# Optimization experiments

Hardware: AMD Instinct MI355X
Metric: run time of the kernel (lower is better)

## Reference

```python
import jax, jax.numpy as jnp
import numpy as np

NUM_ATOMS = 100000
NUM_BONDS = 200000
MAX_NB = 6
ATOM_FDIM = 133
BOND_FDIM = 147
HIDDEN = 300
DEPTH = 4
NUM_MOLS = 8192


def setup_inputs() -> dict:
    key = jax.random.key(0)
    ks = jax.random.split(key, 10)
    f_atoms = jax.random.normal(ks[0], (NUM_ATOMS, ATOM_FDIM), dtype=jnp.float32)
    f_bonds = jax.random.normal(ks[1], (NUM_BONDS, BOND_FDIM), dtype=jnp.float32)
    a2b = jax.random.randint(ks[2], (NUM_ATOMS, MAX_NB), 0, NUM_BONDS, dtype=jnp.int32)
    b2a = jax.random.randint(ks[3], (NUM_BONDS,), 0, NUM_ATOMS, dtype=jnp.int32)
    b2revb = jax.random.randint(ks[4], (NUM_BONDS,), 0, NUM_BONDS, dtype=jnp.int32)
    mol_ids = jnp.sort(jax.random.randint(ks[5], (NUM_ATOMS,), 0, NUM_MOLS, dtype=jnp.int32))
    s = 1.0 / np.sqrt(HIDDEN)
    W_i = jax.random.uniform(ks[6], (BOND_FDIM, HIDDEN), jnp.float32, -s, s)
    W_h = jax.random.uniform(ks[7], (HIDDEN, HIDDEN), jnp.float32, -s, s)
    W_o = jax.random.uniform(ks[8], (ATOM_FDIM + HIDDEN, HIDDEN), jnp.float32, -s, s)
    b_o = jax.random.uniform(ks[9], (HIDDEN,), jnp.float32, -s, s)
    return {"f_atoms": f_atoms, "f_bonds": f_bonds, "W_i": W_i, "W_h": W_h,
            "W_o": W_o, "b_o": b_o, "a2b": a2b, "b2a": b2a, "b2revb": b2revb,
            "mol_ids": mol_ids}


def reference(f_atoms, f_bonds, W_i, W_h, W_o, b_o, a2b, b2a, b2revb, mol_ids):
    # initial bond messages: W_i then activation (bias=False)
    inp = f_bonds @ W_i                       # [B, H]
    message = jax.nn.relu(inp)
    for _ in range(DEPTH - 1):
        nei = message[a2b]                    # [A, MAX_NB, H] gather
        a_message = nei.sum(axis=1)           # [A, H]
        rev_message = message[b2revb]         # [B, H]
        message = a_message[b2a] - rev_message
        message = jax.nn.relu(inp + message @ W_h)
    # final atom readout
    a_message = message[a2b].sum(axis=1)      # [A, H]
    a_input = jnp.concatenate([f_atoms, a_message], axis=1)
    atom_hiddens = jax.nn.relu(a_input @ W_o + b_o)
    # per-molecule mean aggregation (== chemprop a_scope loop with 'mean')
    sums = jax.ops.segment_sum(atom_hiddens, mol_ids, num_segments=NUM_MOLS)
    counts = jax.ops.segment_sum(jnp.ones((NUM_ATOMS,), jnp.float32), mol_ids,
                                 num_segments=NUM_MOLS)
    return sums / jnp.maximum(counts, 1.0)[:, None]
```

## Files before the change

### kernel.cpp

```cpp
#include <hip/hip_runtime.h>


#define DEVFN static __device__ __forceinline__

typedef __attribute__((ext_vector_type(8))) __bf16 bf16x8;
typedef __attribute__((ext_vector_type(4))) float floatx4;

DEVFN unsigned short f2bf(float f) {
    unsigned int u = __float_as_uint(f);
    u += 0x7FFFu + ((u >> 16) & 1u);
    return (unsigned short)(u >> 16);
}
DEVFN float bf2f(unsigned int u) { return __uint_as_float(u << 16); }

DEVFN unsigned int bfsub2(unsigned int a, unsigned int m) {
    float lo = bf2f(a & 0xffffu) - bf2f(m & 0xffffu);
    float hi = bf2f(a >> 16) - bf2f(m >> 16);
    return (unsigned int)f2bf(lo) | ((unsigned int)f2bf(hi) << 16);
}
DEVFN uint4 bfsub8(uint4 a, uint4 m) {
    return make_uint4(bfsub2(a.x, m.x), bfsub2(a.y, m.y),
                      bfsub2(a.z, m.z), bfsub2(a.w, m.w));
}

__global__ __launch_bounds__(256) void dbg_fill(float* out, int n, float v) {
    int t = blockIdx.x * 256 + threadIdx.x;
    if (t < n) out[t] = v;
}

__global__ __launch_bounds__(256) void prep_wih(const float* __restrict__ Wi,
                                                const float* __restrict__ Wh,
                                                unsigned short* __restrict__ Wt) {
    int t = blockIdx.x * 256 + threadIdx.x;
    if (t >= 320 * 480) return;
    int n = t / 480, k = t - n * 480;
    float v = 0.f;
    if (n < 300) {
        if (k < 147) v = Wi[k * 300 + n];
        else if (k >= 160 && k < 460) v = Wh[(k - 160) * 300 + n];
    }
    Wt[t] = f2bf(v);
}

__global__ __launch_bounds__(256) void prep_wto(const float* __restrict__ Wo,
                                                unsigned short* __restrict__ Wt) {
    int t = blockIdx.x * 256 + threadIdx.x;
    if (t >= 320 * 448) return;
    int n = t / 448, k = t - n * 448;
    float v = 0.f;
    if (n < 300) {
        if (k < 300) v = Wo[(133 + k) * 300 + n];
        else if (k >= 304 && k < 437) v = Wo[(k - 304) * 300 + n];
    }
    Wt[t] = f2bf(v);
}

__global__ __launch_bounds__(256) void pad_bonds(const float* __restrict__ fb,
                                                 unsigned short* __restrict__ out) {
    int t = blockIdx.x * 256 + threadIdx.x;
    if (t >= 200000 * 20) return;
    int b = t / 20, c = t - b * 20;
    unsigned int o[4];
#pragma unroll
    for (int p = 0; p < 4; ++p) {
        int sc = c * 8 + p * 2;
        float v0 = (sc < 147) ? fb[(size_t)b * 147 + sc] : 0.f;
        float v1 = (sc + 1 < 147) ? fb[(size_t)b * 147 + sc + 1] : 0.f;
        o[p] = (unsigned int)f2bf(v0) | ((unsigned int)f2bf(v1) << 16);
    }
    *(uint4*)(out + (size_t)b * 160 + c * 8) = make_uint4(o[0], o[1], o[2], o[3]);
}

__global__ __launch_bounds__(256) void atoms_concat(const float* __restrict__ fa,
                                                    unsigned short* __restrict__ concat) {
    int t = blockIdx.x * 256 + threadIdx.x;
    if (t >= 100000 * 18) return;
    int a = t / 18, c = t - a * 18;
    unsigned int o[4];
#pragma unroll
    for (int p = 0; p < 4; ++p) {
        int sc = c * 8 + p * 2;
        float v0 = (sc < 133) ? fa[(size_t)a * 133 + sc] : 0.f;
        float v1 = (sc + 1 < 133) ? fa[(size_t)a * 133 + sc + 1] : 0.f;
        o[p] = (unsigned int)f2bf(v0) | ((unsigned int)f2bf(v1) << 16);
    }
    *(uint4*)(concat + (size_t)a * 448 + 304 + c * 8) = make_uint4(o[0], o[1], o[2], o[3]);
}

template <int CH>
__global__ __launch_bounds__(256) void gather_sum(const unsigned short* __restrict__ msg,
                                                  const int* __restrict__ a2b,
                                                  unsigned short* __restrict__ out,
                                                  int ostride, int nA) {
    int t = blockIdx.x * 256 + threadIdx.x;
    if (t >= nA * CH) return;
    int a = t / CH, c = t - a * CH;
    float s[8] = {0, 0, 0, 0, 0, 0, 0, 0};
#pragma unroll
    for (int j = 0; j < 6; ++j) {
        int b = a2b[a * 6 + j];
        uint4 v = *(const uint4*)(msg + (size_t)b * 320 + c * 8);
        s[0] += bf2f(v.x & 0xffffu); s[1] += bf2f(v.x >> 16);
        s[2] += bf2f(v.y & 0xffffu); s[3] += bf2f(v.y >> 16);
        s[4] += bf2f(v.z & 0xffffu); s[5] += bf2f(v.z >> 16);
        s[6] += bf2f(v.w & 0xffffu); s[7] += bf2f(v.w >> 16);
    }
    unsigned int o[4];
#pragma unroll
    for (int p = 0; p < 4; ++p)
        o[p] = (unsigned int)f2bf(s[2 * p]) | ((unsigned int)f2bf(s[2 * p + 1]) << 16);
    *(uint4*)(out + (size_t)a * ostride + c * 8) = make_uint4(o[0], o[1], o[2], o[3]);
}

template <int KT0, int KT1, int MODE, int BSTRIDE>
__global__ __launch_bounds__(256) void gemm_k(const unsigned short* __restrict__ A0,
                                              int a0s,
                                              const unsigned short* __restrict__ amsg,
                                              const unsigned short* __restrict__ msg,
                                              const int* __restrict__ b2a,
                                              const int* __restrict__ b2revb,
                                              const unsigned short* __restrict__ Wt,
                                              unsigned short* __restrict__ outp,
                                              float* __restrict__ hid,
                                              const float* __restrict__ bo, int M) {
    constexpr int KT = KT0 + KT1;
    __shared__ unsigned short As[2 * 5120];
    __shared__ unsigned short Bs[2 * 5120];

    const int tid = threadIdx.x;
    const int lane = tid & 63;
    const int wave = tid >> 6;
    const int wm = wave & 1, wn = wave >> 1;
    const int l16 = lane & 15, quad = lane >> 4;

    int m0, n0;
    {
        const int bid = blockIdx.x;
        const int MB = (int)(gridDim.x >> 1);
        const int mfull = (MB >> 3) << 3;
        const int FULL = mfull << 1;
        int mb, nh;
        if (bid < FULL) {
            nh = (bid >> 3) & 1;
            mb = ((bid >> 4) << 3) + (bid & 7);
        } else {
            const int r = bid - FULL;
            const int rem = MB - mfull;
            nh = (r >= rem) ? 1 : 0;
            mb = mfull + r - nh * rem;
        }
        m0 = mb * 128;
        n0 = nh * 160;
    }

    const int arow = tid >> 1, ahalf = tid & 1;
    const int gr = min(m0 + arow, M - 1);
    const unsigned short* a0p = A0 + (size_t)gr * a0s + ahalf * 16;
    const unsigned short* a1p = nullptr;
    const unsigned short* m1p = nullptr;
    if (KT1 > 0) {
        a1p = amsg + (size_t)b2a[gr] * 320 + ahalf * 16;
        m1p = msg + (size_t)b2revb[gr] * 320 + ahalf * 16;
    }
    const int u0 = tid, u1 = tid + 256, u2 = tid + 512;
    const unsigned short* bg0 = Wt + (size_t)(n0 + (u0 >> 2)) * BSTRIDE + ((u0 ^ (u0 >> 2)) & 3) * 8;
    const unsigned short* bg1 = Wt + (size_t)(n0 + (u1 >> 2)) * BSTRIDE + ((u1 ^ (u1 >> 2)) & 3) * 8;
    const unsigned short* bg2 = (tid < 128)
        ? Wt + (size_t)(n0 + (u2 >> 2)) * BSTRIDE + ((u2 ^ (u2 >> 2)) & 3) * 8 : Wt;

    int aoff[4], boff[5];
#pragma unroll
    for (int tm = 0; tm < 4; ++tm)
        aoff[tm] = (wm * 64 + tm * 16 + l16) * 40 + quad * 8;
#pragma unroll
    for (int tn = 0; tn < 5; ++tn) {
        int nl = wn * 80 + tn * 16 + l16;
        boff[tn] = nl * 32 + ((quad ^ nl) & 3) * 8;
    }

    floatx4 acc[4][5];
#pragma unroll
    for (int tm = 0; tm < 4; ++tm)
#pragma unroll
        for (int tn = 0; tn < 5; ++tn) acc[tm][tn] = (floatx4){0.f, 0.f, 0.f, 0.f};

    uint4 ar0, ar1, br0, br1, br2;
    auto ldG = [&](int kt) {
        if (kt < KT0) {
            ar0 = *(const uint4*)(a0p + kt * 32);
            ar1 = *(const uint4*)(a0p + kt * 32 + 8);
        } else {
            int ko = (kt - KT0) * 32;
            uint4 va0 = *(const uint4*)(a1p + ko);
            uint4 va1 = *(const uint4*)(a1p + ko + 8);
            uint4 vm0 = *(const uint4*)(m1p + ko);
            uint4 vm1 = *(const uint4*)(m1p + ko + 8);
            ar0 = bfsub8(va0, vm0);
            ar1 = bfsub8(va1, vm1);
        }
        br0 = *(const uint4*)(bg0 + kt * 32);
        br1 = *(const uint4*)(bg1 + kt * 32);
        if (tid < 128) br2 = *(const uint4*)(bg2 + kt * 32);
    };
    auto stW = [&](int buf) {
        unsigned short* ab = As + buf * 5120 + arow * 40 + ahalf * 16;
        *(uint4*)(ab) = ar0;
        *(uint4*)(ab + 8) = ar1;
        unsigned short* bb = Bs + buf * 5120;
        *(uint4*)(bb + u0 * 8) = br0;
        *(uint4*)(bb + u1 * 8) = br1;
        if (tid < 128) *(uint4*)(bb + u2 * 8) = br2;
    };

    ldG(0);
    stW(0);
    __syncthreads();

#pragma unroll
    for (int kt = 0; kt < KT; ++kt) {
        const int buf = kt & 1;
        if (kt + 1 < KT) ldG(kt + 1);

        bf16x8 av[4], bv[5];
#pragma unroll
        for (int tm = 0; tm < 4; ++tm)
            av[tm] = *(const bf16x8*)(As + buf * 5120 + aoff[tm]);
#pragma unroll
        for (int tn = 0; tn < 5; ++tn)
            bv[tn] = *(const bf16x8*)(Bs + buf * 5120 + boff[tn]);
#pragma unroll
        for (int tn = 0; tn < 5; ++tn)
#pragma unroll
            for (int tm = 0; tm < 4; ++tm)
                acc[tm][tn] = __builtin_amdgcn_mfma_f32_16x16x32_bf16(av[tm], bv[tn], acc[tm][tn], 0, 0, 0);

        if (kt + 1 < KT) stW(buf ^ 1);
        __syncthreads();
    }

    float bias[5];
    if (MODE == 2) {
#pragma unroll
        for (int tn = 0; tn < 5; ++tn) {
            int col = n0 + wn * 80 + tn * 16 + l16;
            bias[tn] = (col < 300) ? bo[col] : 0.f;
        }
    }
#pragma unroll
    for (int tm = 0; tm < 4; ++tm) {
        const int r0 = m0 + wm * 64 + tm * 16 + quad * 4;
#pragma unroll
        for (int tn = 0; tn < 5; ++tn) {
            const int col = n0 + wn * 80 + tn * 16 + l16;
#pragma unroll
            for (int i = 0; i < 4; ++i) {
                int r = r0 + i;
                if (r >= M) continue;
                float c = acc[tm][tn][i];
                if (MODE == 2) {
                    if (col < 300) hid[(size_t)r * 300 + col] = fmaxf(c + bias[tn], 0.f);
                } else {
                    outp[(size_t)r * 320 + col] = f2bf(fmaxf(c, 0.f));
                }
            }
        }
    }
}

__global__ __launch_bounds__(320) void mean_k(const float* __restrict__ hid,
                                              const int* __restrict__ mol_ids,
                                              float* __restrict__ out, int nA) {
    int mol = blockIdx.x;
    int lo, hi;
    {
        int l = 0, h = nA;
        while (l < h) { int m = (l + h) >> 1; if (mol_ids[m] < mol) l = m + 1; else h = m; }
        lo = l;
    }
    {
        int l = lo, h = nA;
        while (l < h) { int m = (l + h) >> 1; if (mol_ids[m] < mol + 1) l = m + 1; else h = m; }
        hi = l;
    }
    int col = threadIdx.x;
    if (col >= 300) return;
    float s = 0.f;
    for (int a = lo; a < hi; ++a) s += hid[(size_t)a * 300 + col];
    int cnt = hi - lo;
    out[(size_t)mol * 300 + col] = s / (float)(cnt > 0 ? cnt : 1);
}

extern "C" void kernel_launch(void* const* d_in, const int* in_sizes, int n_in,
                              void* d_out, int out_size, void* d_ws, size_t ws_size,
                              hipStream_t stream) {
    (void)in_sizes; (void)n_in;
    const float* f_atoms = (const float*)d_in[0];
    const float* f_bonds = (const float*)d_in[1];
    const float* W_i     = (const float*)d_in[2];
    const float* W_h     = (const float*)d_in[3];
    const float* W_o     = (const float*)d_in[4];
    const float* b_o     = (const float*)d_in[5];
    const int*   a2b     = (const int*)d_in[6];
    const int*   b2a     = (const int*)d_in[7];
    const int*   b2revb  = (const int*)d_in[8];
    const int*   mol_ids = (const int*)d_in[9];

    const size_t sz_wih  = 320ull * 480 * 2;
    const size_t sz_wto  = 320ull * 448 * 2;
    const size_t sz_fbp  = 200000ull * 160 * 2;
    const size_t sz_amsg = 100000ull * 320 * 2;
    const size_t sz_msg  = 200000ull * 320 * 2;
    const size_t need = sz_wih + sz_wto + sz_fbp + sz_amsg + 2 * sz_msg;

    if (ws_size < need) {
        dbg_fill<<<(out_size + 255) / 256, 256, 0, stream>>>(
            (float*)d_out, out_size, (float)(ws_size >> 20));
        return;
    }

    char* ws = (char*)d_ws;
    unsigned short* wih  = (unsigned short*)(ws);
    unsigned short* wto  = (unsigned short*)(ws + sz_wih);
    unsigned short* fbp  = (unsigned short*)(ws + sz_wih + sz_wto);
    unsigned short* amsg = (unsigned short*)(ws + sz_wih + sz_wto + sz_fbp);
    unsigned short* msgA = (unsigned short*)(ws + sz_wih + sz_wto + sz_fbp + sz_amsg);
    unsigned short* msgB = (unsigned short*)(ws + sz_wih + sz_wto + sz_fbp + sz_amsg + sz_msg);
    unsigned short* concat = msgA;
    float*          hid    = (float*)msgB;

    prep_wih<<<600, 256, 0, stream>>>(W_i, W_h, wih);
    prep_wto<<<560, 256, 0, stream>>>(W_o, wto);
    pad_bonds<<<15625, 256, 0, stream>>>(f_bonds, fbp);

    gemm_k<5, 0, 0, 480><<<dim3(3126), 256, 0, stream>>>(
        fbp, 160, nullptr, nullptr, nullptr, nullptr, wih, msgA, nullptr, nullptr, 200000);

    unsigned short* cur = msgA;
    unsigned short* other = msgB;
    for (int d = 0; d < 3; ++d) {
        gather_sum<40><<<15625, 256, 0, stream>>>(cur, a2b, amsg, 320, 100000);
        gemm_k<5, 10, 0, 480><<<dim3(3126), 256, 0, stream>>>(
            fbp, 160, amsg, cur, b2a, b2revb, wih, other, nullptr, nullptr, 200000);
        unsigned short* t = cur; cur = other; other = t;
    }

    gather_sum<38><<<14844, 256, 0, stream>>>(cur, a2b, concat, 448, 100000);
    atoms_concat<<<7032, 256, 0, stream>>>(f_atoms, concat);
    gemm_k<14, 0, 2, 448><<<dim3(1564), 256, 0, stream>>>(
        concat, 448, nullptr, nullptr, nullptr, nullptr, wto, nullptr, hid, b_o, 100000);
    mean_k<<<8192, 320, 0, stream>>>(hid, mol_ids, (float*)d_out, 100000);
}
```

Measured before the change: 1.167 ms.

## Prefetch global tiles two steps ahead with ping-pong registers in GEMM loop

Deepens the GEMM main-loop software pipeline. Global loads for tile kt+2 are issued into a second register set while tile kt is computed from LDS, so more memory latency is hidden. The __syncthreads is replaced by an explicit lgkmcnt wait, sched barriers and s_barrier. It also drops the trailing barrier after the last tile. This costs extra VGPRs for the second register set, which may lower occupancy.

```diff
diff --git a/kernel.cpp b/kernel.cpp
--- a/kernel.cpp
+++ b/kernel.cpp
@@ -184,43 +184,43 @@
 #pragma unroll
         for (int tn = 0; tn < 5; ++tn) acc[tm][tn] = (floatx4){0.f, 0.f, 0.f, 0.f};
 
-    uint4 ar0, ar1, br0, br1, br2;
-    auto ldG = [&](int kt) {
+    uint4 pa0, pa1, pb0, pb1, pb2;
+    uint4 qa0, qa1, qb0, qb1, qb2;
+
+    auto ldg = [&](int kt, uint4& x0, uint4& x1, uint4& y0, uint4& y1, uint4& y2) {
         if (kt < KT0) {
-            ar0 = *(const uint4*)(a0p + kt * 32);
-            ar1 = *(const uint4*)(a0p + kt * 32 + 8);
+            x0 = *(const uint4*)(a0p + kt * 32);
+            x1 = *(const uint4*)(a0p + kt * 32 + 8);
         } else {
             int ko = (kt - KT0) * 32;
             uint4 va0 = *(const uint4*)(a1p + ko);
             uint4 va1 = *(const uint4*)(a1p + ko + 8);
             uint4 vm0 = *(const uint4*)(m1p + ko);
             uint4 vm1 = *(const uint4*)(m1p + ko + 8);
-            ar0 = bfsub8(va0, vm0);
-            ar1 = bfsub8(va1, vm1);
-        }
-        br0 = *(const uint4*)(bg0 + kt * 32);
-        br1 = *(const uint4*)(bg1 + kt * 32);
-        if (tid < 128) br2 = *(const uint4*)(bg2 + kt * 32);
+            x0 = bfsub8(va0, vm0);
+            x1 = bfsub8(va1, vm1);
+        }
+        y0 = *(const uint4*)(bg0 + kt * 32);
+        y1 = *(const uint4*)(bg1 + kt * 32);
+        if (tid < 128) y2 = *(const uint4*)(bg2 + kt * 32);
     };
-    auto stW = [&](int buf) {
+    auto stw = [&](int buf, const uint4& x0, const uint4& x1,
+                   const uint4& y0, const uint4& y1, const uint4& y2) {
         unsigned short* ab = As + buf * 5120 + arow * 40 + ahalf * 16;
-        *(uint4*)(ab) = ar0;
-        *(uint4*)(ab + 8) = ar1;
+        *(uint4*)(ab) = x0;
+        *(uint4*)(ab + 8) = x1;
         unsigned short* bb = Bs + buf * 5120;
-        *(uint4*)(bb + u0 * 8) = br0;
-        *(uint4*)(bb + u1 * 8) = br1;
-        if (tid < 128) *(uint4*)(bb + u2 * 8) = br2;
+        *(uint4*)(bb + u0 * 8) = y0;
+        *(uint4*)(bb + u1 * 8) = y1;
+        if (tid < 128) *(uint4*)(bb + u2 * 8) = y2;
     };
-
-    ldG(0);
-    stW(0);
-    __syncthreads();
-
-#pragma unroll
-    for (int kt = 0; kt < KT; ++kt) {
-        const int buf = kt & 1;
-        if (kt + 1 < KT) ldG(kt + 1);
-
+    auto barsync = [&]() {
+        asm volatile("s_waitcnt lgkmcnt(0)" ::: "memory");
+        __builtin_amdgcn_sched_barrier(0);
+        __builtin_amdgcn_s_barrier();
+        __builtin_amdgcn_sched_barrier(0);
+    };
+    auto compute = [&](int buf) {
         bf16x8 av[4], bv[5];
 #pragma unroll
         for (int tm = 0; tm < 4; ++tm)
@@ -233,9 +233,24 @@
 #pragma unroll
             for (int tm = 0; tm < 4; ++tm)
                 acc[tm][tn] = __builtin_amdgcn_mfma_f32_16x16x32_bf16(av[tm], bv[tn], acc[tm][tn], 0, 0, 0);
-
-        if (kt + 1 < KT) stW(buf ^ 1);
-        __syncthreads();
+    };
+
+    ldg(0, pa0, pa1, pb0, pb1, pb2);
+    if (KT > 1) ldg(1, qa0, qa1, qb0, qb1, qb2);
+    stw(0, pa0, pa1, pb0, pb1, pb2);
+    barsync();
+
+#pragma unroll
+    for (int kt = 0; kt < KT; ++kt) {
+        if ((kt & 1) == 0) {
+            if (kt + 2 < KT) ldg(kt + 2, pa0, pa1, pb0, pb1, pb2);
+            compute(0);
+            if (kt + 1 < KT) { stw(1, qa0, qa1, qb0, qb1, qb2); barsync(); }
+        } else {
+            if (kt + 2 < KT) ldg(kt + 2, qa0, qa1, qb0, qb1, qb2);
+            compute(1);
+            if (kt + 1 < KT) { stw(0, pa0, pa1, pb0, pb1, pb2); barsync(); }
+        }
     }
 
     float bias[5];
```

After: 1.128 ms. 1.03x faster.

## Load GEMM operands directly into registers, drop LDS staging and fold subtraction into MFMA

Applied to the files above, without the earlier changes.

The GEMM kernel no longer stages A and B tiles through shared memory with barriers. Each wave now loads its MFMA fragments straight from global memory into registers, with a two-deep register prefetch. The a_message minus rev_message subtraction is no longer done in fp32 before bf16 rounding; instead the rev message is sign-flipped and pushed through a second MFMA pass, which doubles MFMA work on the message K-tiles. The launch bounds also request 2 blocks per CU. This removes LDS traffic and syncs, but gives up data reuse across waves (each weight row is fetched by several waves), raises register pressure, and changes the rounding of the subtraction.

```diff
diff --git a/kernel.cpp b/kernel.cpp
--- a/kernel.cpp
+++ b/kernel.cpp
@@ -13,14 +13,9 @@
 }
 DEVFN float bf2f(unsigned int u) { return __uint_as_float(u << 16); }
 
-DEVFN unsigned int bfsub2(unsigned int a, unsigned int m) {
-    float lo = bf2f(a & 0xffffu) - bf2f(m & 0xffffu);
-    float hi = bf2f(a >> 16) - bf2f(m >> 16);
-    return (unsigned int)f2bf(lo) | ((unsigned int)f2bf(hi) << 16);
-}
-DEVFN uint4 bfsub8(uint4 a, uint4 m) {
-    return make_uint4(bfsub2(a.x, m.x), bfsub2(a.y, m.y),
-                      bfsub2(a.z, m.z), bfsub2(a.w, m.w));
+DEVFN uint4 negbf8(uint4 a) {
+    return make_uint4(a.x ^ 0x80008000u, a.y ^ 0x80008000u,
+                      a.z ^ 0x80008000u, a.w ^ 0x80008000u);
 }
 
 __global__ __launch_bounds__(256) void dbg_fill(float* out, int n, float v) {
@@ -113,19 +108,17 @@
 }
 
 template <int KT0, int KT1, int MODE, int BSTRIDE>
-__global__ __launch_bounds__(256) void gemm_k(const unsigned short* __restrict__ A0,
-                                              int a0s,
-                                              const unsigned short* __restrict__ amsg,
-                                              const unsigned short* __restrict__ msg,
-                                              const int* __restrict__ b2a,
-                                              const int* __restrict__ b2revb,
-                                              const unsigned short* __restrict__ Wt,
-                                              unsigned short* __restrict__ outp,
-                                              float* __restrict__ hid,
-                                              const float* __restrict__ bo, int M) {
+__global__ __launch_bounds__(256, 2) void gemm_k(const unsigned short* __restrict__ A0,
+                                                 int a0s,
+                                                 const unsigned short* __restrict__ amsg,
+                                                 const unsigned short* __restrict__ msg,
+                                                 const int* __restrict__ b2a,
+                                                 const int* __restrict__ b2revb,
+                                                 const unsigned short* __restrict__ Wt,
+                                                 unsigned short* __restrict__ outp,
+                                                 float* __restrict__ hid,
+                                                 const float* __restrict__ bo, int M) {
     constexpr int KT = KT0 + KT1;
-    __shared__ unsigned short As[2 * 5120];
-    __shared__ unsigned short Bs[2 * 5120];
 
     const int tid = threadIdx.x;
     const int lane = tid & 63;
@@ -153,89 +146,83 @@
         n0 = nh * 160;
     }
 
-    const int arow = tid >> 1, ahalf = tid & 1;
-    const int gr = min(m0 + arow, M - 1);
-    const unsigned short* a0p = A0 + (size_t)gr * a0s + ahalf * 16;
-    const unsigned short* a1p = nullptr;
-    const unsigned short* m1p = nullptr;
-    if (KT1 > 0) {
-        a1p = amsg + (size_t)b2a[gr] * 320 + ahalf * 16;
-        m1p = msg + (size_t)b2revb[gr] * 320 + ahalf * 16;
-    }
-    const int u0 = tid, u1 = tid + 256, u2 = tid + 512;
-    const unsigned short* bg0 = Wt + (size_t)(n0 + (u0 >> 2)) * BSTRIDE + ((u0 ^ (u0 >> 2)) & 3) * 8;
-    const unsigned short* bg1 = Wt + (size_t)(n0 + (u1 >> 2)) * BSTRIDE + ((u1 ^ (u1 >> 2)) & 3) * 8;
-    const unsigned short* bg2 = (tid < 128)
-        ? Wt + (size_t)(n0 + (u2 >> 2)) * BSTRIDE + ((u2 ^ (u2 >> 2)) & 3) * 8 : Wt;
-
-    int aoff[4], boff[5];
+    const unsigned short* pA0[4];
+    const unsigned short* pA1[4];
+    const unsigned short* pM1[4];
+#pragma unroll
+    for (int tm = 0; tm < 4; ++tm) {
+        const int r = min(m0 + wm * 64 + tm * 16 + l16, M - 1);
+        pA0[tm] = A0 + (size_t)r * a0s + quad * 8;
+        if constexpr (KT1 > 0) {
+            pA1[tm] = amsg + (size_t)b2a[r] * 320 + quad * 8;
+            pM1[tm] = msg + (size_t)b2revb[r] * 320 + quad * 8;
+        } else {
+            pA1[tm] = A0; pM1[tm] = A0;
+        }
+    }
+    const unsigned short* pB[5];
+#pragma unroll
+    for (int tn = 0; tn < 5; ++tn)
+        pB[tn] = Wt + (size_t)(n0 + wn * 80 + tn * 16 + l16) * BSTRIDE + quad * 8;
+
+    floatx4 acc[4][5];
 #pragma unroll
     for (int tm = 0; tm < 4; ++tm)
-        aoff[tm] = (wm * 64 + tm * 16 + l16) * 40 + quad * 8;
-#pragma unroll
-    for (int tn = 0; tn < 5; ++tn) {
-        int nl = wn * 80 + tn * 16 + l16;
-        boff[tn] = nl * 32 + ((quad ^ nl) & 3) * 8;
-    }
-
-    floatx4 acc[4][5];
-#pragma unroll
-    for (int tm = 0; tm < 4; ++tm)
 #pragma unroll
         for (int tn = 0; tn < 5; ++tn) acc[tm][tn] = (floatx4){0.f, 0.f, 0.f, 0.f};
 
-    uint4 ar0, ar1, br0, br1, br2;
-    auto ldG = [&](int kt) {
+    uint4 aP[4], mP[4], bP[5];
+    uint4 aQ[4], mQ[4], bQ[5];
+
+    auto ldg = [&](int kt, uint4 (&a)[4], uint4 (&m)[4], uint4 (&b)[5]) {
         if (kt < KT0) {
-            ar0 = *(const uint4*)(a0p + kt * 32);
-            ar1 = *(const uint4*)(a0p + kt * 32 + 8);
+#pragma unroll
+            for (int tm = 0; tm < 4; ++tm)
+                a[tm] = *(const uint4*)(pA0[tm] + kt * 32);
         } else {
-            int ko = (kt - KT0) * 32;
-            uint4 va0 = *(const uint4*)(a1p + ko);
-            uint4 va1 = *(const uint4*)(a1p + ko + 8);
-            uint4 vm0 = *(const uint4*)(m1p + ko);
-            uint4 vm1 = *(const uint4*)(m1p + ko + 8);
-            ar0 = bfsub8(va0, vm0);
-            ar1 = bfsub8(va1, vm1);
-        }
-        br0 = *(const uint4*)(bg0 + kt * 32);
-        br1 = *(const uint4*)(bg1 + kt * 32);
-        if (tid < 128) br2 = *(const uint4*)(bg2 + kt * 32);
+            const int ko = (kt - KT0) * 32;
+#pragma unroll
+            for (int tm = 0; tm < 4; ++tm) {
+                a[tm] = *(const uint4*)(pA1[tm] + ko);
+                m[tm] = *(const uint4*)(pM1[tm] + ko);
+            }
+        }
+#pragma unroll
+        for (int tn = 0; tn < 5; ++tn)
+            b[tn] = *(const uint4*)(pB[tn] + kt * 32);
     };
-    auto stW = [&](int buf) {
-        unsigned short* ab = As + buf * 5120 + arow * 40 + ahalf * 16;
-        *(uint4*)(ab) = ar0;
-        *(uint4*)(ab + 8) = ar1;
-        unsigned short* bb = Bs + buf * 5120;
-        *(uint4*)(bb + u0 * 8) = br0;
-        *(uint4*)(bb + u1 * 8) = br1;
-        if (tid < 128) *(uint4*)(bb + u2 * 8) = br2;
+    auto mfma_all = [&](const uint4 (&a)[4], const uint4 (&b)[5]) {
+#pragma unroll
+        for (int tn = 0; tn < 5; ++tn)
+#pragma unroll
+            for (int tm = 0; tm < 4; ++tm)
+                acc[tm][tn] = __builtin_amdgcn_mfma_f32_16x16x32_bf16(
+                    __builtin_bit_cast(bf16x8, a[tm]),
+                    __builtin_bit_cast(bf16x8, b[tn]), acc[tm][tn], 0, 0, 0);
     };
-
-    ldG(0);
-    stW(0);
-    __syncthreads();
+    auto step = [&](int kt, const uint4 (&a)[4], const uint4 (&m)[4],
+                    const uint4 (&b)[5]) {
+        mfma_all(a, b);
+        if (kt >= KT0) {
+            uint4 an[4];
+#pragma unroll
+            for (int tm = 0; tm < 4; ++tm) an[tm] = negbf8(m[tm]);
+            mfma_all(an, b);
+        }
+    };
+
+    ldg(0, aP, mP, bP);
+    if (KT > 1) ldg(1, aQ, mQ, bQ);
 
 #pragma unroll
     for (int kt = 0; kt < KT; ++kt) {
-        const int buf = kt & 1;
-        if (kt + 1 < KT) ldG(kt + 1);
-
-        bf16x8 av[4], bv[5];
-#pragma unroll
-        for (int tm = 0; tm < 4; ++tm)
-            av[tm] = *(const bf16x8*)(As + buf * 5120 + aoff[tm]);
-#pragma unroll
-        for (int tn = 0; tn < 5; ++tn)
-            bv[tn] = *(const bf16x8*)(Bs + buf * 5120 + boff[tn]);
-#pragma unroll
-        for (int tn = 0; tn < 5; ++tn)
-#pragma unroll
-            for (int tm = 0; tm < 4; ++tm)
-                acc[tm][tn] = __builtin_amdgcn_mfma_f32_16x16x32_bf16(av[tm], bv[tn], acc[tm][tn], 0, 0, 0);
-
-        if (kt + 1 < KT) stW(buf ^ 1);
-        __syncthreads();
+        if ((kt & 1) == 0) {
+            step(kt, aP, mP, bP);
+            if (kt + 2 < KT) ldg(kt + 2, aP, mP, bP);
+        } else {
+            step(kt, aQ, mQ, bQ);
+            if (kt + 2 < KT) ldg(kt + 2, aQ, mQ, bQ);
+        }
     }
 
     float bias[5];
```

After: 1.585 ms. +35.9%, slower.

## Stage GEMM tiles via direct global-to-LDS loads and fold subtraction into MFMA

Applied to the files above, without the earlier changes.

Replaces the register-staged global loads and LDS stores in the GEMM with global_load_lds direct transfers into swizzled LDS tiles. The a_message minus rev_message subtraction is no longer done in bf16 on load; the reverse message is staged in a separate LDS buffer, sign-flipped, and accumulated with extra MFMAs. This removes register round-trips and the conversion arithmetic but doubles the MFMA work for the message K-range and adds LDS footprint, which may lower occupancy. The two operands are no longer rounded to bf16 after subtracting, so numerics shift slightly.

```diff
diff --git a/kernel.cpp b/kernel.cpp
--- a/kernel.cpp
+++ b/kernel.cpp
@@ -2,6 +2,8 @@
 
 
 #define DEVFN static __device__ __forceinline__
+#define AS1 __attribute__((address_space(1)))
+#define AS3 __attribute__((address_space(3)))
 
 typedef __attribute__((ext_vector_type(8))) __bf16 bf16x8;
 typedef __attribute__((ext_vector_type(4))) float floatx4;
@@ -13,14 +15,9 @@
 }
 DEVFN float bf2f(unsigned int u) { return __uint_as_float(u << 16); }
 
-DEVFN unsigned int bfsub2(unsigned int a, unsigned int m) {
-    float lo = bf2f(a & 0xffffu) - bf2f(m & 0xffffu);
-    float hi = bf2f(a >> 16) - bf2f(m >> 16);
-    return (unsigned int)f2bf(lo) | ((unsigned int)f2bf(hi) << 16);
-}
-DEVFN uint4 bfsub8(uint4 a, uint4 m) {
-    return make_uint4(bfsub2(a.x, m.x), bfsub2(a.y, m.y),
-                      bfsub2(a.z, m.z), bfsub2(a.w, m.w));
+DEVFN void gl16(const unsigned short* g, unsigned short* l) {
+    __builtin_amdgcn_global_load_lds((const AS1 unsigned int*)g,
+                                     (AS3 unsigned int*)l, 16, 0, 0);
 }
 
 __global__ __launch_bounds__(256) void dbg_fill(float* out, int n, float v) {
@@ -124,8 +121,9 @@
                                               float* __restrict__ hid,
                                               const float* __restrict__ bo, int M) {
     constexpr int KT = KT0 + KT1;
-    __shared__ unsigned short As[2 * 5120];
-    __shared__ unsigned short Bs[2 * 5120];
+    __shared__ __align__(16) unsigned short As[2 * 4096];
+    __shared__ __align__(16) unsigned short Bs[2 * 5120];
+    __shared__ __align__(16) unsigned short Ams[(KT1 > 0) ? 2 * 4096 : 64];
 
     const int tid = threadIdx.x;
     const int lane = tid & 63;
@@ -153,25 +151,37 @@
         n0 = nh * 160;
     }
 
-    const int arow = tid >> 1, ahalf = tid & 1;
-    const int gr = min(m0 + arow, M - 1);
-    const unsigned short* a0p = A0 + (size_t)gr * a0s + ahalf * 16;
-    const unsigned short* a1p = nullptr;
-    const unsigned short* m1p = nullptr;
+    const int rl0 = wave * 16 + (lane >> 2);
+    const int rl1 = 64 + rl0;
+    const int csrc = ((lane ^ (lane >> 2)) & 3) * 8;
+    const int gr0 = min(m0 + rl0, M - 1);
+    const int gr1 = min(m0 + rl1, M - 1);
+    const unsigned short* a00 = A0 + (size_t)gr0 * a0s + csrc;
+    const unsigned short* a01 = A0 + (size_t)gr1 * a0s + csrc;
+    const unsigned short* am0 = A0;
+    const unsigned short* am1 = A0;
+    const unsigned short* ms0 = A0;
+    const unsigned short* ms1 = A0;
     if (KT1 > 0) {
-        a1p = amsg + (size_t)b2a[gr] * 320 + ahalf * 16;
-        m1p = msg + (size_t)b2revb[gr] * 320 + ahalf * 16;
+        am0 = amsg + (size_t)b2a[gr0] * 320 + csrc;
+        am1 = amsg + (size_t)b2a[gr1] * 320 + csrc;
+        ms0 = msg + (size_t)b2revb[gr0] * 320 + csrc;
+        ms1 = msg + (size_t)b2revb[gr1] * 320 + csrc;
     }
     const int u0 = tid, u1 = tid + 256, u2 = tid + 512;
-    const unsigned short* bg0 = Wt + (size_t)(n0 + (u0 >> 2)) * BSTRIDE + ((u0 ^ (u0 >> 2)) & 3) * 8;
-    const unsigned short* bg1 = Wt + (size_t)(n0 + (u1 >> 2)) * BSTRIDE + ((u1 ^ (u1 >> 2)) & 3) * 8;
-    const unsigned short* bg2 = (tid < 128)
+    const unsigned short* b0 = Wt + (size_t)(n0 + (u0 >> 2)) * BSTRIDE + ((u0 ^ (u0 >> 2)) & 3) * 8;
+    const unsigned short* b1 = Wt + (size_t)(n0 + (u1 >> 2)) * BSTRIDE + ((u1 ^ (u1 >> 2)) & 3) * 8;
+    const unsigned short* b2 = (tid < 128)
         ? Wt + (size_t)(n0 + (u2 >> 2)) * BSTRIDE + ((u2 ^ (u2 >> 2)) & 3) * 8 : Wt;
 
+    const int aw = wave * 512;
+
     int aoff[4], boff[5];
 #pragma unroll
-    for (int tm = 0; tm < 4; ++tm)
-        aoff[tm] = (wm * 64 + tm * 16 + l16) * 40 + quad * 8;
+    for (int tm = 0; tm < 4; ++tm) {
+        int row = wm * 64 + tm * 16 + l16;
+        aoff[tm] = row * 32 + ((quad ^ row) & 3) * 8;
+    }
 #pragma unroll
     for (int tn = 0; tn < 5; ++tn) {
         int nl = wn * 80 + tn * 16 + l16;
@@ -184,57 +194,67 @@
 #pragma unroll
         for (int tn = 0; tn < 5; ++tn) acc[tm][tn] = (floatx4){0.f, 0.f, 0.f, 0.f};
 
-    uint4 ar0, ar1, br0, br1, br2;
-    auto ldG = [&](int kt) {
+    auto stage = [&](int buf, int kt) {
+        unsigned short* ab = As + buf * 4096;
         if (kt < KT0) {
-            ar0 = *(const uint4*)(a0p + kt * 32);
-            ar1 = *(const uint4*)(a0p + kt * 32 + 8);
+            gl16(a00, ab + aw);
+            gl16(a01, ab + 2048 + aw);
+            if (kt + 1 < KT0) { a00 += 32; a01 += 32; }
         } else {
-            int ko = (kt - KT0) * 32;
-            uint4 va0 = *(const uint4*)(a1p + ko);
-            uint4 va1 = *(const uint4*)(a1p + ko + 8);
-            uint4 vm0 = *(const uint4*)(m1p + ko);
-            uint4 vm1 = *(const uint4*)(m1p + ko + 8);
-            ar0 = bfsub8(va0, vm0);
-            ar1 = bfsub8(va1, vm1);
-        }
-        br0 = *(const uint4*)(bg0 + kt * 32);
-        br1 = *(const uint4*)(bg1 + kt * 32);
-        if (tid < 128) br2 = *(const uint4*)(bg2 + kt * 32);
+            gl16(am0, ab + aw);
+            gl16(am1, ab + 2048 + aw);
+            unsigned short* mb = Ams + buf * 4096;
+            gl16(ms0, mb + aw);
+            gl16(ms1, mb + 2048 + aw);
+            am0 += 32; am1 += 32; ms0 += 32; ms1 += 32;
+        }
+        unsigned short* bb = Bs + buf * 5120;
+        gl16(b0, bb + aw);
+        gl16(b1, bb + 2048 + aw);
+        if (tid < 128) gl16(b2, bb + 4096 + aw);
+        b0 += 32; b1 += 32; b2 += 32;
     };
-    auto stW = [&](int buf) {
-        unsigned short* ab = As + buf * 5120 + arow * 40 + ahalf * 16;
-        *(uint4*)(ab) = ar0;
-        *(uint4*)(ab + 8) = ar1;
-        unsigned short* bb = Bs + buf * 5120;
-        *(uint4*)(bb + u0 * 8) = br0;
-        *(uint4*)(bb + u1 * 8) = br1;
-        if (tid < 128) *(uint4*)(bb + u2 * 8) = br2;
+
+    auto compute = [&](int buf, int kt) {
+        const unsigned short* ab = As + buf * 4096;
+        const unsigned short* bb = Bs + buf * 5120;
+        bf16x8 av[4], bv[5];
+#pragma unroll
+        for (int tm = 0; tm < 4; ++tm)
+            av[tm] = *(const bf16x8*)(ab + aoff[tm]);
+#pragma unroll
+        for (int tn = 0; tn < 5; ++tn)
+            bv[tn] = *(const bf16x8*)(bb + boff[tn]);
+#pragma unroll
+        for (int tn = 0; tn < 5; ++tn)
+#pragma unroll
+            for (int tm = 0; tm < 4; ++tm)
+                acc[tm][tn] = __builtin_amdgcn_mfma_f32_16x16x32_bf16(av[tm], bv[tn], acc[tm][tn], 0, 0, 0);
+        if (kt >= KT0) {
+            const unsigned short* mb = Ams + buf * 4096;
+            bf16x8 mv[4];
+#pragma unroll
+            for (int tm = 0; tm < 4; ++tm) {
+                uint4 u = *(const uint4*)(mb + aoff[tm]);
+                u.x ^= 0x80008000u; u.y ^= 0x80008000u;
+                u.z ^= 0x80008000u; u.w ^= 0x80008000u;
+                mv[tm] = __builtin_bit_cast(bf16x8, u);
+            }
+#pragma unroll
+            for (int tn = 0; tn < 5; ++tn)
+#pragma unroll
+                for (int tm = 0; tm < 4; ++tm)
+                    acc[tm][tn] = __builtin_amdgcn_mfma_f32_16x16x32_bf16(mv[tm], bv[tn], acc[tm][tn], 0, 0, 0);
+        }
     };
 
-    ldG(0);
-    stW(0);
+    stage(0, 0);
     __syncthreads();
-
 #pragma unroll
     for (int kt = 0; kt < KT; ++kt) {
         const int buf = kt & 1;
-        if (kt + 1 < KT) ldG(kt + 1);
-
-        bf16x8 av[4], bv[5];
-#pragma unroll
-        for (int tm = 0; tm < 4; ++tm)
-            av[tm] = *(const bf16x8*)(As + buf * 5120 + aoff[tm]);
-#pragma unroll
-        for (int tn = 0; tn < 5; ++tn)
-            bv[tn] = *(const bf16x8*)(Bs + buf * 5120 + boff[tn]);
-#pragma unroll
-        for (int tn = 0; tn < 5; ++tn)
-#pragma unroll
-            for (int tm = 0; tm < 4; ++tm)
-                acc[tm][tn] = __builtin_amdgcn_mfma_f32_16x16x32_bf16(av[tm], bv[tn], acc[tm][tn], 0, 0, 0);
-
-        if (kt + 1 < KT) stW(buf ^ 1);
+        if (kt + 1 < KT) stage(buf ^ 1, kt + 1);
+        compute(buf, kt);
         __syncthreads();
     }
 
```

Measured after the change: 1.140 ms. 1.02x faster.
